# Kernel tuning notes

Measured on AMD Instinct MI355X. Metric: run time of the kernel, lower is better.

The kernel has to match this reference:

```python
import jax, jax.numpy as jnp
import numpy as np

HEADS = 8
DIM_HEAD = 64
SCALE = DIM_HEAD ** -0.5
LN_EPS = 1e-5
NEG_INF = -1e30


def layernorm(x, gamma, beta):
    mu = jnp.mean(x, axis=-1, keepdims=True)
    var = jnp.var(x, axis=-1, keepdims=True)
    return (x - mu) * jax.lax.rsqrt(var + LN_EPS) * gamma + beta


def setup_inputs() -> dict:
    key = jax.random.key(0)
    ks = jax.random.split(key, 8)
    b, f, n, d, inner = 8, 8192, 64, 1024, HEADS * DIM_HEAD
    x = jax.random.normal(ks[0], (b, f, d), dtype=jnp.float32)
    latents = jax.random.normal(ks[1], (b, n, d), dtype=jnp.float32)
    key_padding_mask = jax.random.randint(ks[2], (b, f), 0, 2) > 0  # True = padded
    s = 0.02
    return {
        "x": x,
        "latents": latents,
        "key_padding_mask": key_padding_mask,
        "kv_gate": jnp.float32(-4.0),
        "gamma_media": jnp.ones((d,), jnp.float32),
        "beta_media": jnp.zeros((d,), jnp.float32),
        "gamma_lat": jnp.ones((d,), jnp.float32),
        "beta_lat": jnp.zeros((d,), jnp.float32),
        "Wq": jax.random.normal(ks[3], (d, inner), jnp.float32) * s,
        "Wk": jax.random.normal(ks[4], (d, inner), jnp.float32) * s,
        "Wv": jax.random.normal(ks[5], (d, inner), jnp.float32) * s,
        "Wout": jax.random.normal(ks[6], (inner, d), jnp.float32) * s,
    }


def reference(x, latents, key_padding_mask, kv_gate, gamma_media, beta_media,
              gamma_lat, beta_lat, Wq, Wk, Wv, Wout):
    b, f, d = x.shape
    n = latents.shape[1]
    x = layernorm(x, gamma_media, beta_media)
    latents = layernorm(latents, gamma_lat, beta_lat)
    kv = jnp.concatenate((x, latents * kv_gate), axis=1)  # (b, f+n, d)

    q = (latents @ Wq).reshape(b, n, HEADS, DIM_HEAD)       # (b, q, h, d)
    k = (kv @ Wk).reshape(b, f + n, HEADS, DIM_HEAD)        # (b, kv, h, d)
    v = (kv @ Wv).reshape(b, f + n, HEADS, DIM_HEAD)

    sim = jnp.einsum('bqhd,bkhd->bhqk', q * SCALE, k)       # (b, h, n, f+n)
    sim = sim - jax.lax.stop_gradient(jnp.max(sim, axis=-1, keepdims=True))

    valid_feat = ~key_padding_mask                          # (b, f)
    valid_full = jnp.concatenate(
        (valid_feat, jnp.ones((b, n), dtype=bool)), axis=1)  # (b, f+n)
    sim = jnp.where(valid_full[:, None, None, :], sim, NEG_INF)

    attn = jax.nn.softmax(sim, axis=-1)
    out = jnp.einsum('bhqk,bkhd->bqhd', attn, v).reshape(b, n, HEADS * DIM_HEAD)
    return out @ Wout
```

## Files before the change

### kernel.cpp

```cpp
#include <hip/hip_runtime.h>
#include <stdint.h>


#define KVPAD 8448
#define NCHUNK 17

typedef __attribute__((ext_vector_type(8))) short short8;
typedef __attribute__((ext_vector_type(4))) float f32x4;

typedef __attribute__((address_space(1))) void gvoid;
typedef __attribute__((address_space(3))) void lvoid;

__device__ __forceinline__ unsigned short f2bf(float f) {
    union { float f; uint32_t u; } v; v.f = f;
    uint32_t u = v.u;
    u += 0x7fffu + ((u >> 16) & 1u);
    return (unsigned short)(u >> 16);
}

__device__ __forceinline__ void mfma16(f32x4& c, short8 a, short8 b) {
    asm volatile("v_mfma_f32_16x16x32_bf16 %0, %1, %2, %0"
                 : "+v"(c) : "v"(a), "v"(b));
}

__device__ __forceinline__ void gl2lds16(const void* g, void* l) {
    __builtin_amdgcn_global_load_lds((gvoid*)g, (lvoid*)l, 16, 0, 0);
}

__global__ __launch_bounds__(1024) void scan_kernel(
    const int* __restrict__ mask, int* __restrict__ pfx, int* __restrict__ cnt)
{
    __shared__ int wsum[16];
    int b = blockIdx.x;
    int t = threadIdx.x, lane = t & 63, w = t >> 6;
    int c[8], tot = 0;
#pragma unroll
    for (int k = 0; k < 8; k++) {
        c[k] = (mask[b * 8192 + k * 1024 + t] == 0) ? 1 : 0;
        tot += c[k];
    }
    int run = tot;
#pragma unroll
    for (int off = 1; off < 64; off <<= 1) {
        int u = __shfl_up(run, off);
        if (lane >= off) run += u;
    }
    if (lane == 63) wsum[w] = run;
    __syncthreads();
    if (t < 16) {
        int v = wsum[t];
#pragma unroll
        for (int off = 1; off < 16; off <<= 1) {
            int u = __shfl_up(v, off);
            if (t >= off) v += u;
        }
        wsum[t] = v;
        if (t == 15) cnt[b] = v;
    }
    __syncthreads();
    int base = (w ? wsum[w - 1] : 0) + (run - tot);
#pragma unroll
    for (int k = 0; k < 8; k++) {
        pfx[b * 8192 + k * 1024 + t] = base;
        base += c[k];
    }
}

__global__ __launch_bounds__(256) void prep_kernel(
    const float* __restrict__ X, const float* __restrict__ latents,
    const int* __restrict__ mask, const int* __restrict__ pfx,
    const float* __restrict__ gm, const float* __restrict__ bm,
    const float* __restrict__ gl, const float* __restrict__ bl,
    const float* __restrict__ Wk, const float* __restrict__ Wv,
    const float* __restrict__ Wq, const float* __restrict__ Wout,
    unsigned short* __restrict__ x_ln, unsigned short* __restrict__ lat_ln,
    unsigned short* __restrict__ WkvqT, unsigned short* __restrict__ WoutT)
{
    __shared__ float t[64][65];
    int blk = blockIdx.x;
    if (blk >= 16512) {
        int tt = blk - 16512;
        int z = tt >> 7, u = tt & 127;
        const float* S; unsigned short* D; int R, C, bx, by;
        if (z == 0)      { S = Wk;   D = WkvqT;                       R = 1024; C = 512;  by = u >> 3; bx = u & 7; }
        else if (z == 1) { S = Wv;   D = WkvqT + (size_t)512 * 1024;  R = 1024; C = 512;  by = u >> 3; bx = u & 7; }
        else if (z == 2) { S = Wq;   D = WkvqT + (size_t)1024 * 1024; R = 1024; C = 512;  by = u >> 3; bx = u & 7; }
        else             { S = Wout; D = WoutT;                       R = 512;  C = 1024; by = u >> 4; bx = u & 15; }
        int r0 = by * 64, c0 = bx * 64;
#pragma unroll
        for (int i = 0; i < 16; i++) {
            int o = i * 256 + threadIdx.x;
            int rr = o >> 6, cc = o & 63;
            t[rr][cc] = S[(size_t)(r0 + rr) * C + c0 + cc];
        }
        __syncthreads();
#pragma unroll
        for (int i = 0; i < 16; i++) {
            int o = i * 256 + threadIdx.x;
            int cl = o >> 6, rl = o & 63;
            D[(size_t)(c0 + cl) * R + r0 + rl] = f2bf(t[rl][cl]);
        }
        return;
    }
    int lane = threadIdx.x & 63;
    int row = blk * 4 + (threadIdx.x >> 6);
    const float *src, *g, *bet;
    unsigned short* dst;
    if (row < 65536) {
        if (mask[row] != 0) return;
        int b = row >> 13;
        src = X + (size_t)row * 1024;
        dst = x_ln + ((size_t)b * 8192 + pfx[row]) * 1024;
        g = gm; bet = bm;
    } else {
        int r = row - 65536;
        src = latents + (size_t)r * 1024;
        dst = lat_ln + (size_t)r * 1024;
        g = gl; bet = bl;
    }
    const float4* xr = (const float4*)src;
    float4 v[4];
    float s = 0.f, s2 = 0.f;
#pragma unroll
    for (int i = 0; i < 4; i++) {
        v[i] = xr[i * 64 + lane];
        s  += v[i].x + v[i].y + v[i].z + v[i].w;
        s2 += v[i].x*v[i].x + v[i].y*v[i].y + v[i].z*v[i].z + v[i].w*v[i].w;
    }
#pragma unroll
    for (int off = 1; off < 64; off <<= 1) {
        s += __shfl_xor(s, off);
        s2 += __shfl_xor(s2, off);
    }
    float mean = s * (1.0f / 1024.0f);
    float var  = s2 * (1.0f / 1024.0f) - mean * mean;
    float rs = rsqrtf(var + 1e-5f);
    ushort4* yr = (ushort4*)dst;
    const float4* gp = (const float4*)g;
    const float4* bp = (const float4*)bet;
#pragma unroll
    for (int i = 0; i < 4; i++) {
        int c4 = i * 64 + lane;
        float4 gg = gp[c4], bb = bp[c4];
        ushort4 o;
        o.x = f2bf((v[i].x - mean) * rs * gg.x + bb.x);
        o.y = f2bf((v[i].y - mean) * rs * gg.y + bb.y);
        o.z = f2bf((v[i].z - mean) * rs * gg.z + bb.z);
        o.w = f2bf((v[i].w - mean) * rs * gg.w + bb.w);
        yr[c4] = o;
    }
}

__global__ __launch_bounds__(256) void gemm_bf16(
    const unsigned short* __restrict__ A, const unsigned short* __restrict__ BT,
    int Kd,
    unsigned short* __restrict__ Ck, float* __restrict__ Cf,
    unsigned short* __restrict__ CvT, unsigned short* __restrict__ Qb,
    int nsplit, int nq, int ldc, int P, int Sstride, int Ofs,
    float scale_const, float qscale, const float* __restrict__ scale_ptr,
    const int* __restrict__ cnt,
    const unsigned short* __restrict__ A2, int latBase)
{
    __shared__ unsigned short a_lds[128 * 64];
    __shared__ unsigned short b_lds[128 * 64];
    int bx = blockIdx.x, by = blockIdx.y;
    bool lat = (latBase > 0 && by >= latBase);
    if (lat) {
        int lid2 = (by - latBase) * 8 + bx;
        bx = lid2 % 12;
        by = lid2 / 12;
        A = A2; nsplit = 512; nq = 1024; ldc = 512;
        P = 64; Sstride = KVPAD; Ofs = 0; cnt = nullptr;
    } else {
        if (latBase > 0) scale_ptr = nullptr;
        if (gridDim.x == 8 && gridDim.y >= 8) {
            int lid = by * 8 + bx;
            bx = lid & 7;
            by = (lid >> 6) * 8 + ((lid >> 3) & 7);
        }
    }
    size_t rowbase = (size_t)by * 128;
    size_t colbase = (size_t)bx * 128;
    if (cnt) {
        int bq = (int)rowbase / P, rl = (int)rowbase - bq * P;
        if (rl >= cnt[bq]) return;
    }
    int tid = threadIdx.x;
    int lane = tid & 63;
    int wave = tid >> 6;
    int wrow = (wave >> 1) * 64, wcol = (wave & 1) * 64;
    int qd = lane >> 4, cc = lane & 15;

    f32x4 acc[4][4];
#pragma unroll
    for (int mt = 0; mt < 4; mt++)
#pragma unroll
        for (int nt = 0; nt < 4; nt++)
            acc[mt][nt] = (f32x4){0.f, 0.f, 0.f, 0.f};

    int kiters = Kd >> 6;
    for (int kt = 0; kt < kiters; kt++) {
        int k0 = kt << 6;
#pragma unroll
        for (int i = 0; i < 4; i++) {
            int s = i * 256 + tid;
            int m = s >> 3, kc = s & 7;
            int kg = kc ^ (m & 7);
            gl2lds16(A + (rowbase + m) * (size_t)Kd + (k0 + kg * 8), &a_lds[s * 8]);
        }
#pragma unroll
        for (int i = 0; i < 4; i++) {
            int s = i * 256 + tid;
            int m = s >> 3, kc = s & 7;
            int kg = kc ^ (m & 7);
            gl2lds16(BT + (colbase + m) * (size_t)Kd + (k0 + kg * 8), &b_lds[s * 8]);
        }
        __syncthreads();
#pragma unroll
        for (int ks = 0; ks < 2; ks++) {
            short8 af[4], bfr[4];
            int cg = ks * 4 + qd;
#pragma unroll
            for (int mt = 0; mt < 4; mt++) {
                int m = wrow + mt * 16 + cc;
                af[mt] = *(const short8*)&a_lds[(m * 8 + (cg ^ (m & 7))) * 8];
            }
#pragma unroll
            for (int nt = 0; nt < 4; nt++) {
                int n = wcol + nt * 16 + cc;
                bfr[nt] = *(const short8*)&b_lds[(n * 8 + (cg ^ (n & 7))) * 8];
            }
#pragma unroll
            for (int mt = 0; mt < 4; mt++)
#pragma unroll
                for (int nt = 0; nt < 4; nt++)
                    mfma16(acc[mt][nt], af[mt], bfr[nt]);
        }
        __syncthreads();
    }

    float sc = scale_const;
    if (scale_ptr) sc *= *scale_ptr;
#pragma unroll
    for (int mt = 0; mt < 4; mt++) {
        int g0 = (int)rowbase + wrow + mt * 16 + qd * 4;
        int bq = g0 / P, rl = g0 - bq * P;
#pragma unroll
        for (int nt = 0; nt < 4; nt++) {
            int col = (int)colbase + wcol + nt * 16 + cc;
            if (col >= nq) {
#pragma unroll
                for (int r = 0; r < 4; r++)
                    Qb[(size_t)(bq * 64 + rl + r) * 512 + (col - nq)] =
                        f2bf(acc[mt][nt][r] * qscale);
            } else if (col < nsplit) {
                int idx0 = bq * Sstride + Ofs + rl;
                if (Cf) {
#pragma unroll
                    for (int r = 0; r < 4; r++)
                        Cf[(size_t)(idx0 + r) * ldc + col] = acc[mt][nt][r] * sc;
                } else {
#pragma unroll
                    for (int r = 0; r < 4; r++)
                        Ck[(size_t)(idx0 + r) * ldc + col] = f2bf(acc[mt][nt][r] * sc);
                }
            } else {
                ushort4 pk;
                pk.x = f2bf(acc[mt][nt][0] * sc);
                pk.y = f2bf(acc[mt][nt][1] * sc);
                pk.z = f2bf(acc[mt][nt][2] * sc);
                pk.w = f2bf(acc[mt][nt][3] * sc);
                *(ushort4*)&CvT[((size_t)bq * 512 + (col - nsplit)) * KVPAD + Ofs + rl] = pk;
            }
        }
    }
}

__global__ __launch_bounds__(256) void attn_kernel(
    const unsigned short* __restrict__ Kbuf,
    const unsigned short* __restrict__ Vt,
    const unsigned short* __restrict__ Qbuf,
    const int* __restrict__ cnt,
    float* __restrict__ Opart,
    float* __restrict__ Mpart,
    float* __restrict__ Lpart)
{
    __shared__ unsigned short P_lds[64 * 264];
    __shared__ float red_max[4][64];
    __shared__ float red_sum[4][64];
    __shared__ float mrow[64];
    __shared__ float lrow[64];
    __shared__ float frow[64];

    int chunk = blockIdx.x, h = blockIdx.y, b = blockIdx.z;
    int len = 64 + cnt[b];
    int kv0 = chunk * 512;
    if (kv0 >= len) return;

    int tid = threadIdx.x, lane = tid & 63, w = tid >> 6;
    int qd = lane >> 4, cc = lane & 15;
    int pidx = (b * 8 + h) * NCHUNK + chunk;

    short8 qf[4][2];
    const unsigned short* Qb = Qbuf + ((size_t)b * 64) * 512 + h * 64;
#pragma unroll
    for (int mt = 0; mt < 4; mt++)
#pragma unroll
        for (int ks = 0; ks < 2; ks++)
            qf[mt][ks] = *(const short8*)&Qb[(size_t)(mt * 16 + cc) * 512 + ks * 32 + qd * 8];

    f32x4 acco[4];
#pragma unroll
    for (int mt = 0; mt < 4; mt++) acco[mt] = (f32x4){0.f, 0.f, 0.f, 0.f};

    const unsigned short* Kb = Kbuf + (size_t)b * KVPAD * 512 + h * 64;
    const unsigned short* Vbase = Vt + ((size_t)b * 512 + h * 64 + w * 16 + cc) * KVPAD;

#pragma unroll 1
    for (int s = 0; s < 2; s++) {
        int kvs = kv0 + s * 256;
        if (kvs >= len) break;
        int kvw = kvs + w * 64;

        f32x4 acc[4][4];
#pragma unroll
        for (int mt = 0; mt < 4; mt++)
#pragma unroll
            for (int nt = 0; nt < 4; nt++)
                acc[mt][nt] = (f32x4){0.f, 0.f, 0.f, 0.f};
#pragma unroll
        for (int nt = 0; nt < 4; nt++) {
            int kvr = kvw + nt * 16 + cc;
#pragma unroll
            for (int ks = 0; ks < 2; ks++) {
                short8 kf = *(const short8*)&Kb[(size_t)kvr * 512 + ks * 32 + qd * 8];
#pragma unroll
                for (int mt = 0; mt < 4; mt++)
                    mfma16(acc[mt][nt], qf[mt][ks], kf);
            }
        }
#pragma unroll
        for (int nt = 0; nt < 4; nt++) {
            int kv = kvw + nt * 16 + cc;
            if (kv >= len) {
#pragma unroll
                for (int mt = 0; mt < 4; mt++)
#pragma unroll
                    for (int r = 0; r < 4; r++) acc[mt][nt][r] = -1e30f;
            }
        }
        float vmax[4][4];
#pragma unroll
        for (int mt = 0; mt < 4; mt++)
#pragma unroll
            for (int r = 0; r < 4; r++)
                vmax[mt][r] = fmaxf(fmaxf(acc[mt][0][r], acc[mt][1][r]),
                                    fmaxf(acc[mt][2][r], acc[mt][3][r]));
#pragma unroll
        for (int off = 1; off < 16; off <<= 1)
#pragma unroll
            for (int mt = 0; mt < 4; mt++)
#pragma unroll
                for (int r = 0; r < 4; r++)
                    vmax[mt][r] = fmaxf(vmax[mt][r], __shfl_xor(vmax[mt][r], off));
        if (cc == 0) {
#pragma unroll
            for (int mt = 0; mt < 4; mt++)
#pragma unroll
                for (int r = 0; r < 4; r++)
                    red_max[w][mt * 16 + qd * 4 + r] = vmax[mt][r];
        }
        __syncthreads();
        if (tid < 64) {
            float tmax = fmaxf(fmaxf(red_max[0][tid], red_max[1][tid]),
                               fmaxf(red_max[2][tid], red_max[3][tid]));
            if (s == 0) {
                mrow[tid] = tmax;
            } else {
                float mo = mrow[tid];
                float mn = fmaxf(mo, tmax);
                frow[tid] = __expf(mo - mn);
                mrow[tid] = mn;
            }
        }
        __syncthreads();
        float vsum[4][4];
#pragma unroll
        for (int mt = 0; mt < 4; mt++)
#pragma unroll
            for (int r = 0; r < 4; r++) {
                int row = mt * 16 + qd * 4 + r;
                float m = mrow[row];
                float ssum = 0.f;
#pragma unroll
                for (int nt = 0; nt < 4; nt++) {
                    float p = __expf(acc[mt][nt][r] - m);
                    ssum += p;
                    P_lds[row * 264 + w * 64 + nt * 16 + cc] = f2bf(p);
                }
                vsum[mt][r] = ssum;
            }
#pragma unroll
        for (int off = 1; off < 16; off <<= 1)
#pragma unroll
            for (int mt = 0; mt < 4; mt++)
#pragma unroll
                for (int r = 0; r < 4; r++)
                    vsum[mt][r] += __shfl_xor(vsum[mt][r], off);
        if (cc == 0) {
#pragma unroll
            for (int mt = 0; mt < 4; mt++)
#pragma unroll
                for (int r = 0; r < 4; r++)
                    red_sum[w][mt * 16 + qd * 4 + r] = vsum[mt][r];
        }
        __syncthreads();
        if (tid < 64) {
            float snew = red_sum[0][tid] + red_sum[1][tid] +
                         red_sum[2][tid] + red_sum[3][tid];
            lrow[tid] = (s == 0) ? snew : lrow[tid] * frow[tid] + snew;
        }
        if (s > 0) {
#pragma unroll
            for (int mt = 0; mt < 4; mt++)
#pragma unroll
                for (int r = 0; r < 4; r++)
                    acco[mt][r] *= frow[mt * 16 + qd * 4 + r];
        }
        const unsigned short* Vb = Vbase + kvs;
#pragma unroll
        for (int ks = 0; ks < 8; ks++) {
            short8 vf = *(const short8*)&Vb[ks * 32 + qd * 8];
#pragma unroll
            for (int mt = 0; mt < 4; mt++) {
                short8 pf = *(const short8*)&P_lds[(size_t)(mt * 16 + cc) * 264 + ks * 32 + qd * 8];
                mfma16(acco[mt], pf, vf);
            }
        }
    }

    if (tid < 64) {
        Mpart[(size_t)pidx * 64 + tid] = mrow[tid];
        Lpart[(size_t)pidx * 64 + tid] = lrow[tid];
    }
    float* Ob = Opart + (size_t)pidx * 4096;
#pragma unroll
    for (int mt = 0; mt < 4; mt++)
#pragma unroll
        for (int r = 0; r < 4; r++)
            Ob[(size_t)(mt * 16 + qd * 4 + r) * 64 + w * 16 + cc] = acco[mt][r];
}

__global__ __launch_bounds__(256) void combine_kernel(
    const float* __restrict__ Opart, const float* __restrict__ Mpart,
    const float* __restrict__ Lpart, const int* __restrict__ cnt,
    unsigned short* __restrict__ AttnOut)
{
    __shared__ float wls[NCHUNK][16];
    __shared__ float invl[16];
    int bh = blockIdx.x >> 2, qg = blockIdx.x & 3;
    int b = bh >> 3, h = bh & 7;
    int pbase = bh * NCHUNK;
    int nact = (64 + cnt[b] + 511) >> 9;
    int tid = threadIdx.x;
    if (tid < 16) {
        int q = qg * 16 + tid;
        float M = -3.0e38f;
        for (int cn = 0; cn < nact; cn++)
            M = fmaxf(M, Mpart[(size_t)(pbase + cn) * 64 + q]);
        float l = 0.f;
        for (int cn = 0; cn < nact; cn++) {
            float wc = __expf(Mpart[(size_t)(pbase + cn) * 64 + q] - M);
            wls[cn][tid] = wc;
            l += wc * Lpart[(size_t)(pbase + cn) * 64 + q];
        }
        invl[tid] = 1.0f / l;
    }
    __syncthreads();
    int ql = tid >> 4, d4 = (tid & 15) * 4;
    int q = qg * 16 + ql;
    float ax = 0.f, ay = 0.f, az = 0.f, aw = 0.f;
    for (int cn = 0; cn < nact; cn++) {
        float wc = wls[cn][ql];
        float4 o = *(const float4*)&Opart[((size_t)(pbase + cn) * 64 + q) * 64 + d4];
        ax += wc * o.x; ay += wc * o.y; az += wc * o.z; aw += wc * o.w;
    }
    float iv = invl[ql];
    ushort4 pk;
    pk.x = f2bf(ax * iv); pk.y = f2bf(ay * iv);
    pk.z = f2bf(az * iv); pk.w = f2bf(aw * iv);
    *(ushort4*)&AttnOut[((size_t)b * 64 + q) * 512 + h * 64 + d4] = pk;
}

#define OPART_OFF    ((size_t)0)
#define MPART_OFF    ((size_t)34603008)
#define LPART_OFF    ((size_t)35143680)
#define XLN_OFF      ((size_t)0)
#define LATLN_OFF    ((size_t)134217728)
#define KBUF_OFF     ((size_t)135266304)
#define VT_OFF       ((size_t)204472320)
#define WKVQT_OFF    ((size_t)273678336)
#define WOUTT_OFF    ((size_t)276824064)
#define PFX_OFF      ((size_t)277872640)
#define CNT_OFF      ((size_t)278134784)
#define QBUF_OFF     ((size_t)278134912)
#define ATTNOUT_OFF  ((size_t)278659200)

extern "C" void kernel_launch(void* const* d_in, const int* in_sizes, int n_in,
                              void* d_out, int out_size, void* d_ws, size_t ws_size,
                              hipStream_t stream) {
    const float* x       = (const float*)d_in[0];
    const float* latents = (const float*)d_in[1];
    const int*   mask    = (const int*)d_in[2];
    const float* kv_gate = (const float*)d_in[3];
    const float* gm      = (const float*)d_in[4];
    const float* bm      = (const float*)d_in[5];
    const float* gl      = (const float*)d_in[6];
    const float* bl      = (const float*)d_in[7];
    const float* Wq      = (const float*)d_in[8];
    const float* Wk      = (const float*)d_in[9];
    const float* Wv      = (const float*)d_in[10];
    const float* Wout    = (const float*)d_in[11];
    float* out = (float*)d_out;

    char* ws = (char*)d_ws;
    float* Opart = (float*)(ws + OPART_OFF);
    float* Mpart = (float*)(ws + MPART_OFF);
    float* Lpart = (float*)(ws + LPART_OFF);
    unsigned short* Qbuf    = (unsigned short*)(ws + QBUF_OFF);
    unsigned short* AttnOut = (unsigned short*)(ws + ATTNOUT_OFF);
    unsigned short* x_ln    = (unsigned short*)(ws + XLN_OFF);
    unsigned short* lat_ln  = (unsigned short*)(ws + LATLN_OFF);
    unsigned short* Kbuf    = (unsigned short*)(ws + KBUF_OFF);
    unsigned short* Vt      = (unsigned short*)(ws + VT_OFF);
    unsigned short* WkvqT   = (unsigned short*)(ws + WKVQT_OFF);
    unsigned short* WoutT   = (unsigned short*)(ws + WOUTT_OFF);
    int* pfx = (int*)(ws + PFX_OFF);
    int* cnt = (int*)(ws + CNT_OFF);

    scan_kernel<<<8, 1024, 0, stream>>>(mask, pfx, cnt);

    prep_kernel<<<17024, 256, 0, stream>>>(
        x, latents, mask, pfx, gm, bm, gl, bl, Wk, Wv, Wq, Wout,
        x_ln, lat_ln, WkvqT, WoutT);

    gemm_bf16<<<dim3(8, 518), 256, 0, stream>>>(
        x_ln, WkvqT, 1024, Kbuf, nullptr, Vt, Qbuf,
        512, 1 << 30, 512, 8192, KVPAD, 64, 1.0f, 0.125f, kv_gate, cnt,
        lat_ln, 512);

    attn_kernel<<<dim3(NCHUNK, 8, 8), 256, 0, stream>>>(
        Kbuf, Vt, Qbuf, cnt, Opart, Mpart, Lpart);

    combine_kernel<<<256, 256, 0, stream>>>(Opart, Mpart, Lpart, cnt, AttnOut);

    gemm_bf16<<<dim3(8, 4), 256, 0, stream>>>(
        AttnOut, WoutT, 512, nullptr, out, nullptr, nullptr,
        1 << 30, 1 << 30, 1024, 64, 64, 0, 1.0f, 0.f, nullptr, nullptr,
        nullptr, 0);
}
```

Measured before the change: 511.5 us.

## Add 256x256 double-buffered KV projection GEMM and split latent GEMM launch

Replaces the merged 128x128-tile GEMM launch for the media K/V projection with a dedicated 256x256-tile, 512-thread kernel. It double-buffers LDS through direct global-to-LDS loads, uses XOR-swizzled layouts and raises wave priority around MFMA bursts. The latent K/V/Q projection moves to its own small launch of the old GEMM, and the merged-grid remapping logic is removed. The larger tiles raise arithmetic intensity and cut LDS/global traffic, at the cost of heavier register use, coarser skipping of padded rows, and one extra kernel launch.

```diff
diff --git a/kernel.cpp b/kernel.cpp
--- a/kernel.cpp
+++ b/kernel.cpp
@@ -26,6 +26,13 @@
 __device__ __forceinline__ void gl2lds16(const void* g, void* l) {
     __builtin_amdgcn_global_load_lds((gvoid*)g, (lvoid*)l, 16, 0, 0);
 }
+
+__device__ __forceinline__ void pbar() {
+    asm volatile("" ::: "memory");
+    __builtin_amdgcn_s_barrier();
+    asm volatile("" ::: "memory");
+}
+#define WAITVM(N) asm volatile("s_waitcnt vmcnt(" #N ")" ::: "memory")
 
 __global__ __launch_bounds__(1024) void scan_kernel(
     const int* __restrict__ mask, int* __restrict__ pfx, int* __restrict__ cnt)
@@ -151,6 +158,165 @@
     }
 }
 
+__global__ __launch_bounds__(512, 2) void gemm256(
+    const unsigned short* __restrict__ A,
+    const unsigned short* __restrict__ BT,
+    unsigned short* __restrict__ Ck,
+    unsigned short* __restrict__ CvT,
+    const int* __restrict__ cnt)
+{
+    __shared__ unsigned short lds[65536];
+    int bx = blockIdx.x, by = blockIdx.y;
+    int lid = by * 4 + bx;
+    lid = (lid & 7) * 128 + (lid >> 3);
+    bx = lid & 3; by = lid >> 2;
+    int rowbase = by * 256;
+    int colbase = bx * 256;
+    int bq = by >> 5;
+    int rl0 = (by & 31) * 256;
+    if (rl0 >= cnt[bq]) return;
+
+    int tid = threadIdx.x;
+    int lane = tid & 63;
+    int wid = tid >> 6;
+    int qd = lane >> 4, cc = lane & 15;
+    int wm = wid >> 2, wn = wid & 3;
+
+    f32x4 acc[8][4];
+#pragma unroll
+    for (int mf = 0; mf < 8; mf++)
+#pragma unroll
+        for (int nf = 0; nf < 4; nf++)
+            acc[mf][nf] = (f32x4){0.f, 0.f, 0.f, 0.f};
+
+#define STAGE_TILE(buf, kt)                                                     \
+    {                                                                           \
+        int bb = (buf) * 32768;                                                 \
+        _Pragma("unroll")                                                       \
+        for (int i = 0; i < 4; i++) {                                           \
+            int s = i * 512 + tid;                                              \
+            int m = s >> 3, kc = s & 7;                                         \
+            int kg = kc ^ (m & 7);                                              \
+            gl2lds16(A + (size_t)(rowbase + m) * 1024 + (kt) * 64 + kg * 8,     \
+                     &lds[bb + s * 8]);                                         \
+        }                                                                       \
+        _Pragma("unroll")                                                       \
+        for (int i = 0; i < 4; i++) {                                           \
+            int s = i * 512 + tid;                                              \
+            int m = s >> 3, kc = s & 7;                                         \
+            int kg = kc ^ (m & 7);                                              \
+            gl2lds16(BT + (size_t)(colbase + m) * 1024 + (kt) * 64 + kg * 8,    \
+                     &lds[bb + 16384 + s * 8]);                                 \
+        }                                                                       \
+    }
+
+    STAGE_TILE(0, 0);
+    WAITVM(0);
+    pbar();
+
+    int cur = 0;
+#pragma unroll 1
+    for (int kt = 0; kt < 16; kt++) {
+        bool pf = (kt < 15);
+        int ab = cur * 32768;
+        int bb = ab + 16384;
+        short8 bf0[4], bf1[4], af[4];
+
+        if (pf) STAGE_TILE(cur ^ 1, kt + 1);
+#pragma unroll
+        for (int nf = 0; nf < 4; nf++) {
+            int n = wn * 64 + nf * 16 + cc;
+            bf0[nf] = *(const short8*)&lds[bb + (n * 8 + (qd ^ (n & 7))) * 8];
+        }
+#pragma unroll
+        for (int i = 0; i < 4; i++) {
+            int m = wm * 128 + i * 16 + cc;
+            af[i] = *(const short8*)&lds[ab + (m * 8 + (qd ^ (m & 7))) * 8];
+        }
+        __builtin_amdgcn_s_setprio(1);
+#pragma unroll
+        for (int i = 0; i < 4; i++)
+#pragma unroll
+            for (int nf = 0; nf < 4; nf++)
+                mfma16(acc[i][nf], af[i], bf0[nf]);
+        __builtin_amdgcn_s_setprio(0);
+        pbar();
+
+#pragma unroll
+        for (int i = 0; i < 4; i++) {
+            int m = wm * 128 + (4 + i) * 16 + cc;
+            af[i] = *(const short8*)&lds[ab + (m * 8 + (qd ^ (m & 7))) * 8];
+        }
+        __builtin_amdgcn_s_setprio(1);
+#pragma unroll
+        for (int i = 0; i < 4; i++)
+#pragma unroll
+            for (int nf = 0; nf < 4; nf++)
+                mfma16(acc[4 + i][nf], af[i], bf0[nf]);
+        __builtin_amdgcn_s_setprio(0);
+        pbar();
+
+#pragma unroll
+        for (int nf = 0; nf < 4; nf++) {
+            int n = wn * 64 + nf * 16 + cc;
+            bf1[nf] = *(const short8*)&lds[bb + (n * 8 + ((4 + qd) ^ (n & 7))) * 8];
+        }
+#pragma unroll
+        for (int i = 0; i < 4; i++) {
+            int m = wm * 128 + i * 16 + cc;
+            af[i] = *(const short8*)&lds[ab + (m * 8 + ((4 + qd) ^ (m & 7))) * 8];
+        }
+        __builtin_amdgcn_s_setprio(1);
+#pragma unroll
+        for (int i = 0; i < 4; i++)
+#pragma unroll
+            for (int nf = 0; nf < 4; nf++)
+                mfma16(acc[i][nf], af[i], bf1[nf]);
+        __builtin_amdgcn_s_setprio(0);
+        pbar();
+
+#pragma unroll
+        for (int i = 0; i < 4; i++) {
+            int m = wm * 128 + (4 + i) * 16 + cc;
+            af[i] = *(const short8*)&lds[ab + (m * 8 + ((4 + qd) ^ (m & 7))) * 8];
+        }
+        __builtin_amdgcn_s_setprio(1);
+#pragma unroll
+        for (int i = 0; i < 4; i++)
+#pragma unroll
+            for (int nf = 0; nf < 4; nf++)
+                mfma16(acc[4 + i][nf], af[i], bf1[nf]);
+        __builtin_amdgcn_s_setprio(0);
+        if (pf) WAITVM(0);
+        pbar();
+        cur ^= 1;
+    }
+#undef STAGE_TILE
+
+    bool isK = (colbase < 512);
+#pragma unroll
+    for (int mf = 0; mf < 8; mf++) {
+        int grow = rl0 + wm * 128 + mf * 16 + qd * 4;
+#pragma unroll
+        for (int nf = 0; nf < 4; nf++) {
+            int col = colbase + wn * 64 + nf * 16 + cc;
+            if (isK) {
+#pragma unroll
+                for (int r = 0; r < 4; r++)
+                    Ck[(size_t)(bq * KVPAD + 64 + grow + r) * 512 + col] =
+                        f2bf(acc[mf][nf][r]);
+            } else {
+                ushort4 pk;
+                pk.x = f2bf(acc[mf][nf][0]);
+                pk.y = f2bf(acc[mf][nf][1]);
+                pk.z = f2bf(acc[mf][nf][2]);
+                pk.w = f2bf(acc[mf][nf][3]);
+                *(ushort4*)&CvT[((size_t)bq * 512 + (col - 512)) * KVPAD + 64 + grow] = pk;
+            }
+        }
+    }
+}
+
 __global__ __launch_bounds__(256) void gemm_bf16(
     const unsigned short* __restrict__ A, const unsigned short* __restrict__ BT,
     int Kd,
@@ -158,27 +324,11 @@
     unsigned short* __restrict__ CvT, unsigned short* __restrict__ Qb,
     int nsplit, int nq, int ldc, int P, int Sstride, int Ofs,
     float scale_const, float qscale, const float* __restrict__ scale_ptr,
-    const int* __restrict__ cnt,
-    const unsigned short* __restrict__ A2, int latBase)
+    const int* __restrict__ cnt)
 {
     __shared__ unsigned short a_lds[128 * 64];
     __shared__ unsigned short b_lds[128 * 64];
     int bx = blockIdx.x, by = blockIdx.y;
-    bool lat = (latBase > 0 && by >= latBase);
-    if (lat) {
-        int lid2 = (by - latBase) * 8 + bx;
-        bx = lid2 % 12;
-        by = lid2 / 12;
-        A = A2; nsplit = 512; nq = 1024; ldc = 512;
-        P = 64; Sstride = KVPAD; Ofs = 0; cnt = nullptr;
-    } else {
-        if (latBase > 0) scale_ptr = nullptr;
-        if (gridDim.x == 8 && gridDim.y >= 8) {
-            int lid = by * 8 + bx;
-            bx = lid & 7;
-            by = (lid >> 6) * 8 + ((lid >> 3) & 7);
-        }
-    }
     size_t rowbase = (size_t)by * 128;
     size_t colbase = (size_t)bx * 128;
     if (cnt) {
@@ -544,10 +694,11 @@
         x, latents, mask, pfx, gm, bm, gl, bl, Wk, Wv, Wq, Wout,
         x_ln, lat_ln, WkvqT, WoutT);
 
-    gemm_bf16<<<dim3(8, 518), 256, 0, stream>>>(
-        x_ln, WkvqT, 1024, Kbuf, nullptr, Vt, Qbuf,
-        512, 1 << 30, 512, 8192, KVPAD, 64, 1.0f, 0.125f, kv_gate, cnt,
-        lat_ln, 512);
+    gemm_bf16<<<dim3(12, 4), 256, 0, stream>>>(
+        lat_ln, WkvqT, 1024, Kbuf, nullptr, Vt, Qbuf,
+        512, 1024, 512, 64, KVPAD, 0, 1.0f, 0.125f, kv_gate, nullptr);
+
+    gemm256<<<dim3(4, 256), 512, 0, stream>>>(x_ln, WkvqT, Kbuf, Vt, cnt);
 
     attn_kernel<<<dim3(NCHUNK, 8, 8), 256, 0, stream>>>(
         Kbuf, Vt, Qbuf, cnt, Opart, Mpart, Lpart);
@@ -556,6 +707,5 @@
 
     gemm_bf16<<<dim3(8, 4), 256, 0, stream>>>(
         AttnOut, WoutT, 512, nullptr, out, nullptr, nullptr,
-        1 << 30, 1 << 30, 1024, 64, 64, 0, 1.0f, 0.f, nullptr, nullptr,
-        nullptr, 0);
-}
+        1 << 30, 1 << 30, 1024, 64, 64, 0, 1.0f, 0.f, nullptr, nullptr);
+}
```

After: 539.3 us. 1.05x slower.
